# Performance work log

Measured on AMD Instinct MI355X. Metric: run time of the kernel, lower is better.

Reference implementation:

```python
import jax, jax.numpy as jnp
import numpy as np

C_IN = 256
GROUP = C_IN // 4  # module hard-codes group = C_in/4 -> 4 channels per group
EPS = 1e-5

@jax.custom_vjp
def binarize(x):
    # 1-bit quantization: sign forward, hardtanh straight-through backward
    return jnp.sign(x)

def _bin_fwd(x):
    return jnp.sign(x), x

def _bin_bwd(x, g):
    return (g * (jnp.abs(x) <= 1.0).astype(g.dtype),)

binarize.defvjp(_bin_fwd, _bin_bwd)

def channel_shuffle(x, g):
    # [N,C,H,W] -> [N,g,C/g,H,W] -> [N,C/g,g,H,W] -> [N,C,H,W]
    N, C, H, W = x.shape
    return x.reshape(N, g, C // g, H, W).transpose(0, 2, 1, 3, 4).reshape(N, C, H, W)


def setup_inputs() -> dict:
    key = jax.random.key(0)
    ks = jax.random.split(key, 6)
    x = jax.random.normal(ks[0], (32, C_IN, 56, 56), jnp.float32)
    # grouped conv weight: [C_out, C_in/group, kH, kW] = [256, 4, 3, 3]
    weight = jax.random.normal(ks[1], (C_IN, C_IN // GROUP, 3, 3), jnp.float32) * 0.1
    gamma = 1.0 + 0.1 * jax.random.normal(ks[2], (C_IN,), jnp.float32)
    beta = 0.1 * jax.random.normal(ks[3], (C_IN,), jnp.float32)
    running_mean = 0.1 * jax.random.normal(ks[4], (C_IN,), jnp.float32)
    running_var = jax.random.uniform(ks[5], (C_IN,), jnp.float32, 0.5, 1.5)
    return dict(x=x, weight=weight, gamma=gamma, beta=beta,
                running_mean=running_mean, running_var=running_var)


def reference(x, weight, gamma, beta, running_mean, running_var):
    # BatchNorm2d (inference-mode, affine=True)
    inv = gamma * jax.lax.rsqrt(running_var + EPS)
    xb = x * inv[None, :, None, None] + (beta - running_mean * inv)[None, :, None, None]
    # Conv2d_1w1a: binarize activations and weights, grouped 3x3 conv, no bias
    a = binarize(xb)
    w = binarize(weight)
    out = jax.lax.conv_general_dilated(
        a, w,
        window_strides=(1, 1),
        padding=((1, 1), (1, 1)),
        dimension_numbers=('NCHW', 'OIHW', 'NCHW'),
        feature_group_count=GROUP,
    )
    out = channel_shuffle(out, GROUP)
    # stride == 1 -> shortcut is identity
    return out + x
```

## Files before the change

kernel.cpp:

```cpp
#include <hip/hip_runtime.h>
#include <stdint.h>

#define H 56
#define W 56
#define HW (H * W)
#define CIN 256
#define IMG (CIN * HW)
#define EPS 1e-5f

#define ROWW 8
#define TROWS 58

__device__ __forceinline__ float mul_rn(float a, float b) {
    float d; asm("v_mul_f32 %0, %1, %2" : "=v"(d) : "v"(a), "v"(b)); return d;
}
__device__ __forceinline__ float add_rn(float a, float b) {
    float d; asm("v_add_f32 %0, %1, %2" : "=v"(d) : "v"(a), "v"(b)); return d;
}
__device__ __forceinline__ float sub_rn(float a, float b) {
    float d; asm("v_sub_f32 %0, %1, %2" : "=v"(d) : "v"(a), "v"(b)); return d;
}

__global__ __launch_bounds__(256)
void binconv_kernel(const float* __restrict__ X,
                    const float* __restrict__ Wt,
                    const float* __restrict__ gamma,
                    const float* __restrict__ beta,
                    const float* __restrict__ mean,
                    const float* __restrict__ var,
                    float* __restrict__ out) {
    __shared__ uint32_t s_tile[TROWS * ROWW];
    __shared__ uint32_t z_tile[TROWS * ROWW];
    __shared__ uint32_t ws_l[4][3];
    __shared__ uint32_t wz_l[4][3];

    const int bx  = blockIdx.x;
    const int n   = bx >> 6;
    const int g   = bx & 63;
    const int tid = threadIdx.x;

    for (int i = tid; i < TROWS * ROWW; i += 256) { s_tile[i] = 0u; z_tile[i] = 0u; }

    if (tid < 4) {
        const float* wc = Wt + (size_t)(g * 4 + tid) * 36;
        for (int r = 0; r < 3; ++r) {
            uint32_t s = 0, z = 0;
            for (int ci = 0; ci < 4; ++ci)
                for (int kw = 0; kw < 3; ++kw) {
                    float v = wc[ci * 9 + r * 3 + kw];
                    int b = kw * 4 + ci;
                    s |= (v > 0.f  ? 1u : 0u) << b;
                    z |= (v != 0.f ? 1u : 0u) << b;
                }
            ws_l[tid][r] = s; wz_l[tid][r] = z;
        }
    }

    float inv[4], bias[4];
#pragma unroll
    for (int ci = 0; ci < 4; ++ci) {
        int c = g * 4 + ci;
        float s  = sqrtf(var[c] + EPS);
        float r  = 1.0f / s;
        float iv = mul_rn(gamma[c], r);
        inv[ci]  = iv;
        bias[ci] = sub_rn(beta[c], mul_rn(mean[c], iv));
    }

    __syncthreads();

    const float* Xn = X + (size_t)n * IMG;

    for (int task = tid; task < 56 * 14; task += 256) {
        int r  = task / 14;
        int cg = task - r * 14;
        int off = r * W + cg * 4;
        uint32_t s16 = 0, z16 = 0;
#pragma unroll
        for (int ci = 0; ci < 4; ++ci) {
            const float4 v = *reinterpret_cast<const float4*>(
                Xn + (size_t)(g * 4 + ci) * HW + off);
            float t0 = add_rn(mul_rn(v.x, inv[ci]), bias[ci]);
            float t1 = add_rn(mul_rn(v.y, inv[ci]), bias[ci]);
            float t2 = add_rn(mul_rn(v.z, inv[ci]), bias[ci]);
            float t3 = add_rn(mul_rn(v.w, inv[ci]), bias[ci]);
            s16 |= ((t0 > 0.f ? 1u : 0u) << ci)        | ((t1 > 0.f ? 1u : 0u) << (4 + ci))
                 | ((t2 > 0.f ? 1u : 0u) << (8 + ci))  | ((t3 > 0.f ? 1u : 0u) << (12 + ci));
            z16 |= ((t0 != 0.f ? 1u : 0u) << ci)       | ((t1 != 0.f ? 1u : 0u) << (4 + ci))
                 | ((t2 != 0.f ? 1u : 0u) << (8 + ci)) | ((t3 != 0.f ? 1u : 0u) << (12 + ci));
        }
        reinterpret_cast<uint16_t*>(&s_tile[(r + 1) * ROWW])[cg] = (uint16_t)s16;
        reinterpret_cast<uint16_t*>(&z_tile[(r + 1) * ROWW])[cg] = (uint16_t)z16;
    }

    __syncthreads();

    uint32_t wsj[4][3], wzj[4][3];
    bool full = true;
#pragma unroll
    for (int j = 0; j < 4; ++j)
#pragma unroll
        for (int r = 0; r < 3; ++r) {
            wsj[j][r] = ws_l[j][r];
            wzj[j][r] = wz_l[j][r];
            full = full && (wzj[j][r] == 0xFFFu);
        }

    float* On = out + (size_t)n * IMG;

    for (int task = tid; task < 56 * 14; task += 256) {
        int h  = task / 14;
        int cg = task - h * 14;
        int w0 = cg * 4;

        uint64_t vs[3], vz[3];
        int off;
        if (w0 == 0) {
            off = 0;
#pragma unroll
            for (int r = 0; r < 3; ++r) {
                int base = (h + r) * ROWW;
                vs[r] = (((uint64_t)s_tile[base] | ((uint64_t)s_tile[base + 1] << 32)) << 4);
                vz[r] = (((uint64_t)z_tile[base] | ((uint64_t)z_tile[base + 1] << 32)) << 4);
            }
        } else {
            int st = 4 * w0 - 4;
            int i0 = st >> 5;
            off = st & 31;
#pragma unroll
            for (int r = 0; r < 3; ++r) {
                int base = (h + r) * ROWW + i0;
                vs[r] = ((uint64_t)s_tile[base] | ((uint64_t)s_tile[base + 1] << 32));
                vz[r] = ((uint64_t)z_tile[base] | ((uint64_t)z_tile[base + 1] << 32));
            }
        }

        int res[4][4];
        if (full) {
#pragma unroll
            for (int k = 0; k < 4; ++k) {
                int sh = off + 4 * k;
                uint32_t s0 = (uint32_t)(vs[0] >> sh) & 0xFFFu;
                uint32_t s1 = (uint32_t)(vs[1] >> sh) & 0xFFFu;
                uint32_t s2 = (uint32_t)(vs[2] >> sh) & 0xFFFu;
                uint32_t z0 = (uint32_t)(vz[0] >> sh) & 0xFFFu;
                uint32_t z1 = (uint32_t)(vz[1] >> sh) & 0xFFFu;
                uint32_t z2 = (uint32_t)(vz[2] >> sh) & 0xFFFu;
                int vb = __popc(z0) + __popc(z1) + __popc(z2);
#pragma unroll
                for (int j = 0; j < 4; ++j) {
                    int pc = __popc((s0 ^ wsj[j][0]) & z0)
                           + __popc((s1 ^ wsj[j][1]) & z1)
                           + __popc((s2 ^ wsj[j][2]) & z2);
                    res[j][k] = vb - 2 * pc;
                }
            }
        } else {
#pragma unroll
            for (int k = 0; k < 4; ++k) {
                int sh = off + 4 * k;
                uint32_t s0 = (uint32_t)(vs[0] >> sh) & 0xFFFu;
                uint32_t s1 = (uint32_t)(vs[1] >> sh) & 0xFFFu;
                uint32_t s2 = (uint32_t)(vs[2] >> sh) & 0xFFFu;
                uint32_t z0 = (uint32_t)(vz[0] >> sh) & 0xFFFu;
                uint32_t z1 = (uint32_t)(vz[1] >> sh) & 0xFFFu;
                uint32_t z2 = (uint32_t)(vz[2] >> sh) & 0xFFFu;
#pragma unroll
                for (int j = 0; j < 4; ++j) {
                    uint32_t m0 = z0 & wzj[j][0];
                    uint32_t m1 = z1 & wzj[j][1];
                    uint32_t m2 = z2 & wzj[j][2];
                    int vb = __popc(m0) + __popc(m1) + __popc(m2);
                    int pc = __popc((s0 ^ wsj[j][0]) & m0)
                           + __popc((s1 ^ wsj[j][1]) & m1)
                           + __popc((s2 ^ wsj[j][2]) & m2);
                    res[j][k] = vb - 2 * pc;
                }
            }
        }

        size_t pbase = (size_t)h * W + w0;
#pragma unroll
        for (int j = 0; j < 4; ++j) {
            size_t cofs = (size_t)(j * 64 + g) * HW + pbase;
            const float4 sc = *reinterpret_cast<const float4*>(Xn + cofs);
            float4 o;
            o.x = add_rn((float)res[j][0], sc.x);
            o.y = add_rn((float)res[j][1], sc.y);
            o.z = add_rn((float)res[j][2], sc.z);
            o.w = add_rn((float)res[j][3], sc.w);
            *reinterpret_cast<float4*>(On + cofs) = o;
        }
    }
}

extern "C" void kernel_launch(void* const* d_in, const int* in_sizes, int n_in,
                              void* d_out, int out_size, void* d_ws, size_t ws_size,
                              hipStream_t stream) {
    const float* X     = (const float*)d_in[0];
    const float* Wt    = (const float*)d_in[1];
    const float* gamma = (const float*)d_in[2];
    const float* beta  = (const float*)d_in[3];
    const float* mean  = (const float*)d_in[4];
    const float* var   = (const float*)d_in[5];
    float* out = (float*)d_out;

    int N = in_sizes[0] / IMG;

    binconv_kernel<<<N * 64, 256, 0, stream>>>(X, Wt, gamma, beta, mean, var, out);
}
```

Before: 206.0 us.

## Process two images per block with register-prefetched loads overlapping compute

Each block now handles two batch images for the same channel group, using double-buffered shared bit tiles. The second image's activations are loaded into registers before the first image's convolution runs, so global load latency overlaps the popcount work. Residual loads are hoisted ahead of the bit math, weight masks are made wave-uniform with readfirstlane, and launch bounds request 4 blocks per CU. In exchange the grid is halved, register pressure rises, and an odd batch size would leave one image unprocessed.

```diff
diff --git a/kernel.cpp b/kernel.cpp
--- a/kernel.cpp
+++ b/kernel.cpp
@@ -10,6 +10,7 @@
 
 #define ROWW 8
 #define TROWS 58
+#define TILE_SZ (TROWS * ROWW)
 
 __device__ __forceinline__ float mul_rn(float a, float b) {
     float d; asm("v_mul_f32 %0, %1, %2" : "=v"(d) : "v"(a), "v"(b)); return d;
@@ -21,25 +22,184 @@
     float d; asm("v_sub_f32 %0, %1, %2" : "=v"(d) : "v"(a), "v"(b)); return d;
 }
 
-__global__ __launch_bounds__(256)
+
+__device__ __forceinline__ void stage_issue(const float* __restrict__ Xn, int g, int tid,
+                                            float4 v[3][4]) {
+#pragma unroll
+    for (int i = 0; i < 3; ++i) {
+        int t   = tid + i * 256;
+        int r   = t / 14;
+        int cg  = t - r * 14;
+        int off = r * W + cg * 4;
+#pragma unroll
+        for (int ci = 0; ci < 4; ++ci)
+            v[i][ci] = *reinterpret_cast<const float4*>(Xn + (size_t)(g * 4 + ci) * HW + off);
+    }
+}
+
+__device__ __forceinline__ void bn_pack(const float4 q[4], const float inv[4], const float bias[4],
+                                        uint32_t& s16, uint32_t& z16) {
+    s16 = 0u; z16 = 0u;
+#pragma unroll
+    for (int ci = 0; ci < 4; ++ci) {
+        float t0 = add_rn(mul_rn(q[ci].x, inv[ci]), bias[ci]);
+        float t1 = add_rn(mul_rn(q[ci].y, inv[ci]), bias[ci]);
+        float t2 = add_rn(mul_rn(q[ci].z, inv[ci]), bias[ci]);
+        float t3 = add_rn(mul_rn(q[ci].w, inv[ci]), bias[ci]);
+        s16 |= ((t0 > 0.f ? 1u : 0u) << ci)        | ((t1 > 0.f ? 1u : 0u) << (4 + ci))
+             | ((t2 > 0.f ? 1u : 0u) << (8 + ci))  | ((t3 > 0.f ? 1u : 0u) << (12 + ci));
+        z16 |= ((t0 != 0.f ? 1u : 0u) << ci)       | ((t1 != 0.f ? 1u : 0u) << (4 + ci))
+             | ((t2 != 0.f ? 1u : 0u) << (8 + ci)) | ((t3 != 0.f ? 1u : 0u) << (12 + ci));
+    }
+}
+
+__device__ __forceinline__ void stage_convert(const float4 v[3][4], const float inv[4],
+                                              const float bias[4],
+                                              uint32_t* s_t, uint32_t* z_t,
+                                              int tid, const float* __restrict__ Xn, int g) {
+#pragma unroll
+    for (int i = 0; i < 3; ++i) {
+        int t  = tid + i * 256;
+        int r  = t / 14;
+        int cg = t - r * 14;
+        uint32_t s16, z16;
+        bn_pack(v[i], inv, bias, s16, z16);
+        reinterpret_cast<uint16_t*>(&s_t[(r + 1) * ROWW])[cg] = (uint16_t)s16;
+        reinterpret_cast<uint16_t*>(&z_t[(r + 1) * ROWW])[cg] = (uint16_t)z16;
+    }
+    if (tid < 16) {
+        int t   = 768 + tid;
+        int r   = t / 14;
+        int cg  = t - r * 14;
+        int off = r * W + cg * 4;
+        float4 q[4];
+#pragma unroll
+        for (int ci = 0; ci < 4; ++ci)
+            q[ci] = *reinterpret_cast<const float4*>(Xn + (size_t)(g * 4 + ci) * HW + off);
+        uint32_t s16, z16;
+        bn_pack(q, inv, bias, s16, z16);
+        reinterpret_cast<uint16_t*>(&s_t[(r + 1) * ROWW])[cg] = (uint16_t)s16;
+        reinterpret_cast<uint16_t*>(&z_t[(r + 1) * ROWW])[cg] = (uint16_t)z16;
+    }
+}
+
+__device__ __forceinline__ void phaseB(const uint32_t* s_t, const uint32_t* z_t,
+                                       const float* __restrict__ Xn, float* __restrict__ On,
+                                       int g, int tid,
+                                       const uint32_t wsj[4][3], const uint32_t wzj[4][3],
+                                       bool full) {
+    for (int task = tid; task < 56 * 14; task += 256) {
+        int h  = task / 14;
+        int cg = task - h * 14;
+        int w0 = cg * 4;
+        size_t pbase = (size_t)h * W + w0;
+
+        float4 sc[4];
+#pragma unroll
+        for (int j = 0; j < 4; ++j)
+            sc[j] = *reinterpret_cast<const float4*>(Xn + (size_t)(j * 64 + g) * HW + pbase);
+
+        uint64_t vs[3], vz[3];
+        int off;
+        if (w0 == 0) {
+            off = 0;
+#pragma unroll
+            for (int r = 0; r < 3; ++r) {
+                int base = (h + r) * ROWW;
+                vs[r] = (((uint64_t)s_t[base] | ((uint64_t)s_t[base + 1] << 32)) << 4);
+                vz[r] = (((uint64_t)z_t[base] | ((uint64_t)z_t[base + 1] << 32)) << 4);
+            }
+        } else {
+            int st = 4 * w0 - 4;
+            int i0 = st >> 5;
+            off = st & 31;
+#pragma unroll
+            for (int r = 0; r < 3; ++r) {
+                int base = (h + r) * ROWW + i0;
+                vs[r] = ((uint64_t)s_t[base] | ((uint64_t)s_t[base + 1] << 32));
+                vz[r] = ((uint64_t)z_t[base] | ((uint64_t)z_t[base + 1] << 32));
+            }
+        }
+
+        int res[4][4];
+        if (full) {
+#pragma unroll
+            for (int k = 0; k < 4; ++k) {
+                int sh = off + 4 * k;
+                uint32_t s0 = (uint32_t)(vs[0] >> sh) & 0xFFFu;
+                uint32_t s1 = (uint32_t)(vs[1] >> sh) & 0xFFFu;
+                uint32_t s2 = (uint32_t)(vs[2] >> sh) & 0xFFFu;
+                uint32_t z0 = (uint32_t)(vz[0] >> sh) & 0xFFFu;
+                uint32_t z1 = (uint32_t)(vz[1] >> sh) & 0xFFFu;
+                uint32_t z2 = (uint32_t)(vz[2] >> sh) & 0xFFFu;
+                int vb = __popc(z0) + __popc(z1) + __popc(z2);
+#pragma unroll
+                for (int j = 0; j < 4; ++j) {
+                    int pc = __popc((s0 ^ wsj[j][0]) & z0)
+                           + __popc((s1 ^ wsj[j][1]) & z1)
+                           + __popc((s2 ^ wsj[j][2]) & z2);
+                    res[j][k] = vb - 2 * pc;
+                }
+            }
+        } else {
+#pragma unroll
+            for (int k = 0; k < 4; ++k) {
+                int sh = off + 4 * k;
+                uint32_t s0 = (uint32_t)(vs[0] >> sh) & 0xFFFu;
+                uint32_t s1 = (uint32_t)(vs[1] >> sh) & 0xFFFu;
+                uint32_t s2 = (uint32_t)(vs[2] >> sh) & 0xFFFu;
+                uint32_t z0 = (uint32_t)(vz[0] >> sh) & 0xFFFu;
+                uint32_t z1 = (uint32_t)(vz[1] >> sh) & 0xFFFu;
+                uint32_t z2 = (uint32_t)(vz[2] >> sh) & 0xFFFu;
+#pragma unroll
+                for (int j = 0; j < 4; ++j) {
+                    uint32_t m0 = z0 & wzj[j][0];
+                    uint32_t m1 = z1 & wzj[j][1];
+                    uint32_t m2 = z2 & wzj[j][2];
+                    int vb = __popc(m0) + __popc(m1) + __popc(m2);
+                    int pc = __popc((s0 ^ wsj[j][0]) & m0)
+                           + __popc((s1 ^ wsj[j][1]) & m1)
+                           + __popc((s2 ^ wsj[j][2]) & m2);
+                    res[j][k] = vb - 2 * pc;
+                }
+            }
+        }
+
+#pragma unroll
+        for (int j = 0; j < 4; ++j) {
+            size_t cofs = (size_t)(j * 64 + g) * HW + pbase;
+            float4 o;
+            o.x = add_rn((float)res[j][0], sc[j].x);
+            o.y = add_rn((float)res[j][1], sc[j].y);
+            o.z = add_rn((float)res[j][2], sc[j].z);
+            o.w = add_rn((float)res[j][3], sc[j].w);
+            *reinterpret_cast<float4*>(On + cofs) = o;
+        }
+    }
+}
+
+__global__ __launch_bounds__(256, 4)
 void binconv_kernel(const float* __restrict__ X,
                     const float* __restrict__ Wt,
                     const float* __restrict__ gamma,
                     const float* __restrict__ beta,
                     const float* __restrict__ mean,
                     const float* __restrict__ var,
-                    float* __restrict__ out) {
-    __shared__ uint32_t s_tile[TROWS * ROWW];
-    __shared__ uint32_t z_tile[TROWS * ROWW];
+                    float* __restrict__ out, int nHalf) {
+    __shared__ uint32_t s_tile[2][TILE_SZ];
+    __shared__ uint32_t z_tile[2][TILE_SZ];
     __shared__ uint32_t ws_l[4][3];
     __shared__ uint32_t wz_l[4][3];
 
     const int bx  = blockIdx.x;
-    const int n   = bx >> 6;
+    const int n0  = bx >> 6;
     const int g   = bx & 63;
     const int tid = threadIdx.x;
 
-    for (int i = tid; i < TROWS * ROWW; i += 256) { s_tile[i] = 0u; z_tile[i] = 0u; }
+    for (int i = tid; i < 2 * TILE_SZ; i += 256) {
+        (&s_tile[0][0])[i] = 0u;
+        (&z_tile[0][0])[i] = 0u;
+    }
 
     if (tid < 4) {
         const float* wc = Wt + (size_t)(g * 4 + tid) * 36;
@@ -67,33 +227,17 @@
         bias[ci] = sub_rn(beta[c], mul_rn(mean[c], iv));
     }
 
+    const float* Xn0 = X   + (size_t)n0 * IMG;
+    const float* Xn1 = X   + (size_t)(n0 + nHalf) * IMG;
+    float*       On0 = out + (size_t)n0 * IMG;
+    float*       On1 = out + (size_t)(n0 + nHalf) * IMG;
+
+    float4 v0[3][4];
+    stage_issue(Xn0, g, tid, v0);
+
     __syncthreads();
 
-    const float* Xn = X + (size_t)n * IMG;
-
-    for (int task = tid; task < 56 * 14; task += 256) {
-        int r  = task / 14;
-        int cg = task - r * 14;
-        int off = r * W + cg * 4;
-        uint32_t s16 = 0, z16 = 0;
-#pragma unroll
-        for (int ci = 0; ci < 4; ++ci) {
-            const float4 v = *reinterpret_cast<const float4*>(
-                Xn + (size_t)(g * 4 + ci) * HW + off);
-            float t0 = add_rn(mul_rn(v.x, inv[ci]), bias[ci]);
-            float t1 = add_rn(mul_rn(v.y, inv[ci]), bias[ci]);
-            float t2 = add_rn(mul_rn(v.z, inv[ci]), bias[ci]);
-            float t3 = add_rn(mul_rn(v.w, inv[ci]), bias[ci]);
-            s16 |= ((t0 > 0.f ? 1u : 0u) << ci)        | ((t1 > 0.f ? 1u : 0u) << (4 + ci))
-                 | ((t2 > 0.f ? 1u : 0u) << (8 + ci))  | ((t3 > 0.f ? 1u : 0u) << (12 + ci));
-            z16 |= ((t0 != 0.f ? 1u : 0u) << ci)       | ((t1 != 0.f ? 1u : 0u) << (4 + ci))
-                 | ((t2 != 0.f ? 1u : 0u) << (8 + ci)) | ((t3 != 0.f ? 1u : 0u) << (12 + ci));
-        }
-        reinterpret_cast<uint16_t*>(&s_tile[(r + 1) * ROWW])[cg] = (uint16_t)s16;
-        reinterpret_cast<uint16_t*>(&z_tile[(r + 1) * ROWW])[cg] = (uint16_t)z16;
-    }
-
-    __syncthreads();
+    stage_convert(v0, inv, bias, s_tile[0], z_tile[0], tid, Xn0, g);
 
     uint32_t wsj[4][3], wzj[4][3];
     bool full = true;
@@ -101,97 +245,23 @@
     for (int j = 0; j < 4; ++j)
 #pragma unroll
         for (int r = 0; r < 3; ++r) {
-            wsj[j][r] = ws_l[j][r];
-            wzj[j][r] = wz_l[j][r];
+            wsj[j][r] = __builtin_amdgcn_readfirstlane(ws_l[j][r]);
+            wzj[j][r] = __builtin_amdgcn_readfirstlane(wz_l[j][r]);
             full = full && (wzj[j][r] == 0xFFFu);
         }
 
-    float* On = out + (size_t)n * IMG;
-
-    for (int task = tid; task < 56 * 14; task += 256) {
-        int h  = task / 14;
-        int cg = task - h * 14;
-        int w0 = cg * 4;
-
-        uint64_t vs[3], vz[3];
-        int off;
-        if (w0 == 0) {
-            off = 0;
-#pragma unroll
-            for (int r = 0; r < 3; ++r) {
-                int base = (h + r) * ROWW;
-                vs[r] = (((uint64_t)s_tile[base] | ((uint64_t)s_tile[base + 1] << 32)) << 4);
-                vz[r] = (((uint64_t)z_tile[base] | ((uint64_t)z_tile[base + 1] << 32)) << 4);
-            }
-        } else {
-            int st = 4 * w0 - 4;
-            int i0 = st >> 5;
-            off = st & 31;
-#pragma unroll
-            for (int r = 0; r < 3; ++r) {
-                int base = (h + r) * ROWW + i0;
-                vs[r] = ((uint64_t)s_tile[base] | ((uint64_t)s_tile[base + 1] << 32));
-                vz[r] = ((uint64_t)z_tile[base] | ((uint64_t)z_tile[base + 1] << 32));
-            }
-        }
-
-        int res[4][4];
-        if (full) {
-#pragma unroll
-            for (int k = 0; k < 4; ++k) {
-                int sh = off + 4 * k;
-                uint32_t s0 = (uint32_t)(vs[0] >> sh) & 0xFFFu;
-                uint32_t s1 = (uint32_t)(vs[1] >> sh) & 0xFFFu;
-                uint32_t s2 = (uint32_t)(vs[2] >> sh) & 0xFFFu;
-                uint32_t z0 = (uint32_t)(vz[0] >> sh) & 0xFFFu;
-                uint32_t z1 = (uint32_t)(vz[1] >> sh) & 0xFFFu;
-                uint32_t z2 = (uint32_t)(vz[2] >> sh) & 0xFFFu;
-                int vb = __popc(z0) + __popc(z1) + __popc(z2);
-#pragma unroll
-                for (int j = 0; j < 4; ++j) {
-                    int pc = __popc((s0 ^ wsj[j][0]) & z0)
-                           + __popc((s1 ^ wsj[j][1]) & z1)
-                           + __popc((s2 ^ wsj[j][2]) & z2);
-                    res[j][k] = vb - 2 * pc;
-                }
-            }
-        } else {
-#pragma unroll
-            for (int k = 0; k < 4; ++k) {
-                int sh = off + 4 * k;
-                uint32_t s0 = (uint32_t)(vs[0] >> sh) & 0xFFFu;
-                uint32_t s1 = (uint32_t)(vs[1] >> sh) & 0xFFFu;
-                uint32_t s2 = (uint32_t)(vs[2] >> sh) & 0xFFFu;
-                uint32_t z0 = (uint32_t)(vz[0] >> sh) & 0xFFFu;
-                uint32_t z1 = (uint32_t)(vz[1] >> sh) & 0xFFFu;
-                uint32_t z2 = (uint32_t)(vz[2] >> sh) & 0xFFFu;
-#pragma unroll
-                for (int j = 0; j < 4; ++j) {
-                    uint32_t m0 = z0 & wzj[j][0];
-                    uint32_t m1 = z1 & wzj[j][1];
-                    uint32_t m2 = z2 & wzj[j][2];
-                    int vb = __popc(m0) + __popc(m1) + __popc(m2);
-                    int pc = __popc((s0 ^ wsj[j][0]) & m0)
-                           + __popc((s1 ^ wsj[j][1]) & m1)
-                           + __popc((s2 ^ wsj[j][2]) & m2);
-                    res[j][k] = vb - 2 * pc;
-                }
-            }
-        }
-
-        size_t pbase = (size_t)h * W + w0;
-#pragma unroll
-        for (int j = 0; j < 4; ++j) {
-            size_t cofs = (size_t)(j * 64 + g) * HW + pbase;
-            const float4 sc = *reinterpret_cast<const float4*>(Xn + cofs);
-            float4 o;
-            o.x = add_rn((float)res[j][0], sc.x);
-            o.y = add_rn((float)res[j][1], sc.y);
-            o.z = add_rn((float)res[j][2], sc.z);
-            o.w = add_rn((float)res[j][3], sc.w);
-            *reinterpret_cast<float4*>(On + cofs) = o;
-        }
-    }
+    __syncthreads();
+
+    float4 v1[3][4];
+    stage_issue(Xn1, g, tid, v1);
+
+    phaseB(s_tile[0], z_tile[0], Xn0, On0, g, tid, wsj, wzj, full);
+
+    stage_convert(v1, inv, bias, s_tile[1], z_tile[1], tid, Xn1, g);
+
+    __syncthreads();
+
+    phaseB(s_tile[1], z_tile[1], Xn1, On1, g, tid, wsj, wzj, full);
 }
 
 extern "C" void kernel_launch(void* const* d_in, const int* in_sizes, int n_in,
@@ -205,7 +275,8 @@
     const float* var   = (const float*)d_in[5];
     float* out = (float*)d_out;
 
-    int N = in_sizes[0] / IMG;
-
-    binconv_kernel<<<N * 64, 256, 0, stream>>>(X, Wt, gamma, beta, mean, var, out);
-}
+    int N     = in_sizes[0] / IMG;
+    int nHalf = N >> 1;
+
+    binconv_kernel<<<nHalf * 64, 256, 0, stream>>>(X, Wt, gamma, beta, mean, var, out, nHalf);
+}
```

Measured after the change: 198.7 us. 1.04x faster.

## Split each image-group block into two row halves and hoist shortcut loads

Applied to the files above, without the earlier changes.

Doubles the grid by assigning each block half of the image rows for one channel group, recomputing a one-row halo of binarized activations. BN scale/bias and weight masks are moved into scalar registers via readfirstlane, and residual loads are issued before the popcount work to overlap latency. The aim is more parallelism and better latency hiding at the cost of slightly redundant halo loads and per-block setup.

```diff
diff --git a/kernel.cpp b/kernel.cpp
--- a/kernel.cpp
+++ b/kernel.cpp
@@ -9,7 +9,10 @@
 #define EPS 1e-5f
 
 #define ROWW 8
-#define TROWS 58
+#define TR2 30
+#define TSZ (TR2 * ROWW)
+#define ATASKS 406
+#define BTASKS 392
 
 __device__ __forceinline__ float mul_rn(float a, float b) {
     float d; asm("v_mul_f32 %0, %1, %2" : "=v"(d) : "v"(a), "v"(b)); return d;
@@ -20,6 +23,16 @@
 __device__ __forceinline__ float sub_rn(float a, float b) {
     float d; asm("v_sub_f32 %0, %1, %2" : "=v"(d) : "v"(a), "v"(b)); return d;
 }
+__device__ __forceinline__ float mul_rn_sv(float s, float v) {
+    float d; asm("v_mul_f32 %0, %1, %2" : "=v"(d) : "s"(s), "v"(v)); return d;
+}
+__device__ __forceinline__ float add_rn_sv(float s, float v) {
+    float d; asm("v_add_f32 %0, %1, %2" : "=v"(d) : "s"(s), "v"(v)); return d;
+}
+__device__ __forceinline__ float rfl_f(float x) {
+    return __int_as_float(__builtin_amdgcn_readfirstlane(__float_as_int(x)));
+}
+
 
 __global__ __launch_bounds__(256)
 void binconv_kernel(const float* __restrict__ X,
@@ -29,17 +42,21 @@
                     const float* __restrict__ mean,
                     const float* __restrict__ var,
                     float* __restrict__ out) {
-    __shared__ uint32_t s_tile[TROWS * ROWW];
-    __shared__ uint32_t z_tile[TROWS * ROWW];
+    __shared__ uint32_t s_tile[TSZ];
+    __shared__ uint32_t z_tile[TSZ];
     __shared__ uint32_t ws_l[4][3];
     __shared__ uint32_t wz_l[4][3];
 
-    const int bx  = blockIdx.x;
-    const int n   = bx >> 6;
-    const int g   = bx & 63;
-    const int tid = threadIdx.x;
-
-    for (int i = tid; i < TROWS * ROWW; i += 256) { s_tile[i] = 0u; z_tile[i] = 0u; }
+    const int bx   = blockIdx.x;
+    const int half = bx & 1;
+    const int g    = (bx >> 1) & 63;
+    const int n    = bx >> 7;
+    const int tid  = threadIdx.x;
+
+    for (int i = tid; i < 2 * TSZ; i += 256) {
+        if (i < TSZ) s_tile[i] = 0u;
+        else         z_tile[i - TSZ] = 0u;
+    }
 
     if (tid < 4) {
         const float* wc = Wt + (size_t)(g * 4 + tid) * 36;
@@ -63,37 +80,39 @@
         float s  = sqrtf(var[c] + EPS);
         float r  = 1.0f / s;
         float iv = mul_rn(gamma[c], r);
-        inv[ci]  = iv;
-        bias[ci] = sub_rn(beta[c], mul_rn(mean[c], iv));
-    }
+        inv[ci]  = rfl_f(iv);
+        bias[ci] = rfl_f(sub_rn(beta[c], mul_rn(mean[c], iv)));
+    }
+
+    const float* Xn = X   + (size_t)n * IMG;
+    float*       On = out + (size_t)n * IMG;
 
     __syncthreads();
 
-    const float* Xn = X + (size_t)n * IMG;
-
-    for (int task = tid; task < 56 * 14; task += 256) {
-        int r  = task / 14;
-        int cg = task - r * 14;
-        int off = r * W + cg * 4;
+    const int rowbase = half * 27;
+    const int rtoff   = 1 - half;
+    for (int task = tid; task < ATASKS; task += 256) {
+        int ar = task / 14;
+        int cg = task - ar * 14;
+        int off = (rowbase + ar) * W + cg * 4;
         uint32_t s16 = 0, z16 = 0;
 #pragma unroll
         for (int ci = 0; ci < 4; ++ci) {
             const float4 v = *reinterpret_cast<const float4*>(
                 Xn + (size_t)(g * 4 + ci) * HW + off);
-            float t0 = add_rn(mul_rn(v.x, inv[ci]), bias[ci]);
-            float t1 = add_rn(mul_rn(v.y, inv[ci]), bias[ci]);
-            float t2 = add_rn(mul_rn(v.z, inv[ci]), bias[ci]);
-            float t3 = add_rn(mul_rn(v.w, inv[ci]), bias[ci]);
+            float t0 = add_rn_sv(bias[ci], mul_rn_sv(inv[ci], v.x));
+            float t1 = add_rn_sv(bias[ci], mul_rn_sv(inv[ci], v.y));
+            float t2 = add_rn_sv(bias[ci], mul_rn_sv(inv[ci], v.z));
+            float t3 = add_rn_sv(bias[ci], mul_rn_sv(inv[ci], v.w));
             s16 |= ((t0 > 0.f ? 1u : 0u) << ci)        | ((t1 > 0.f ? 1u : 0u) << (4 + ci))
                  | ((t2 > 0.f ? 1u : 0u) << (8 + ci))  | ((t3 > 0.f ? 1u : 0u) << (12 + ci));
             z16 |= ((t0 != 0.f ? 1u : 0u) << ci)       | ((t1 != 0.f ? 1u : 0u) << (4 + ci))
                  | ((t2 != 0.f ? 1u : 0u) << (8 + ci)) | ((t3 != 0.f ? 1u : 0u) << (12 + ci));
         }
-        reinterpret_cast<uint16_t*>(&s_tile[(r + 1) * ROWW])[cg] = (uint16_t)s16;
-        reinterpret_cast<uint16_t*>(&z_tile[(r + 1) * ROWW])[cg] = (uint16_t)z16;
-    }
-
-    __syncthreads();
+        int rt = ar + rtoff;
+        reinterpret_cast<uint16_t*>(&s_tile[rt * ROWW])[cg] = (uint16_t)s16;
+        reinterpret_cast<uint16_t*>(&z_tile[rt * ROWW])[cg] = (uint16_t)z16;
+    }
 
     uint32_t wsj[4][3], wzj[4][3];
     bool full = true;
@@ -101,17 +120,18 @@
     for (int j = 0; j < 4; ++j)
 #pragma unroll
         for (int r = 0; r < 3; ++r) {
-            wsj[j][r] = ws_l[j][r];
-            wzj[j][r] = wz_l[j][r];
+            wsj[j][r] = __builtin_amdgcn_readfirstlane(ws_l[j][r]);
+            wzj[j][r] = __builtin_amdgcn_readfirstlane(wz_l[j][r]);
             full = full && (wzj[j][r] == 0xFFFu);
         }
 
-    float* On = out + (size_t)n * IMG;
-
-    for (int task = tid; task < 56 * 14; task += 256) {
-        int h  = task / 14;
-        int cg = task - h * 14;
+    __syncthreads();
+
+    for (int task = tid; task < BTASKS; task += 256) {
+        int hl = task / 14;
+        int cg = task - hl * 14;
         int w0 = cg * 4;
+        size_t pbase = (size_t)(half * 28 + hl) * W + w0;
 
         uint64_t vs[3], vz[3];
         int off;
@@ -119,7 +139,7 @@
             off = 0;
 #pragma unroll
             for (int r = 0; r < 3; ++r) {
-                int base = (h + r) * ROWW;
+                int base = (hl + r) * ROWW;
                 vs[r] = (((uint64_t)s_tile[base] | ((uint64_t)s_tile[base + 1] << 32)) << 4);
                 vz[r] = (((uint64_t)z_tile[base] | ((uint64_t)z_tile[base + 1] << 32)) << 4);
             }
@@ -129,11 +149,16 @@
             off = st & 31;
 #pragma unroll
             for (int r = 0; r < 3; ++r) {
-                int base = (h + r) * ROWW + i0;
+                int base = (hl + r) * ROWW + i0;
                 vs[r] = ((uint64_t)s_tile[base] | ((uint64_t)s_tile[base + 1] << 32));
                 vz[r] = ((uint64_t)z_tile[base] | ((uint64_t)z_tile[base + 1] << 32));
             }
         }
+
+        float4 sc[4];
+#pragma unroll
+        for (int j = 0; j < 4; ++j)
+            sc[j] = *reinterpret_cast<const float4*>(Xn + (size_t)(j * 64 + g) * HW + pbase);
 
         int res[4][4];
         if (full) {
@@ -179,16 +204,14 @@
             }
         }
 
-        size_t pbase = (size_t)h * W + w0;
 #pragma unroll
         for (int j = 0; j < 4; ++j) {
             size_t cofs = (size_t)(j * 64 + g) * HW + pbase;
-            const float4 sc = *reinterpret_cast<const float4*>(Xn + cofs);
             float4 o;
-            o.x = add_rn((float)res[j][0], sc.x);
-            o.y = add_rn((float)res[j][1], sc.y);
-            o.z = add_rn((float)res[j][2], sc.z);
-            o.w = add_rn((float)res[j][3], sc.w);
+            o.x = add_rn((float)res[j][0], sc[j].x);
+            o.y = add_rn((float)res[j][1], sc[j].y);
+            o.z = add_rn((float)res[j][2], sc[j].z);
+            o.w = add_rn((float)res[j][3], sc[j].w);
             *reinterpret_cast<float4*>(On + cofs) = o;
         }
     }
@@ -207,5 +230,5 @@
 
     int N = in_sizes[0] / IMG;
 
-    binconv_kernel<<<N * 64, 256, 0, stream>>>(X, Wt, gamma, beta, mean, var, out);
-}
+    binconv_kernel<<<N * 64 * 2, 256, 0, stream>>>(X, Wt, gamma, beta, mean, var, out);
+}
```

Result: faster. 201.5 us (-2.2%).
